# Kernel optimization log

Hardware: AMD Instinct MI355X
Metric: run time of the kernel (lower is better)

The kernel has to match this reference:

```python
import jax, jax.numpy as jnp
import numpy as np

DIM = 128      # channels C
HEADS = 4
HD = DIM // HEADS  # head_dim = 32
N = 128        # window tokens = 2*8*8
BW = 2048      # B_ = batch * num_windows
NP = 256       # sp_mask partitions
NW = 256       # shift-mask windows
TABLE = 675    # (2*2-1)*(2*8-1)*(2*8-1)
SCALE = HD ** -0.5


def setup_inputs() -> dict:
    key = jax.random.key(0)
    ks = jax.random.split(key, 8)
    x = jax.random.normal(ks[0], (BW, N, DIM), jnp.float32)
    rpi = jax.random.randint(ks[1], (N, N), 0, TABLE, dtype=jnp.int32)
    mask = jax.random.normal(ks[2], (NW, N, N), jnp.float32)
    sp_mask = jax.random.normal(ks[3], (NP, N, N), jnp.float32)
    w_qkv = jax.random.normal(ks[4], (3 * DIM, DIM), jnp.float32) * 0.02
    b_qkv = jnp.zeros((3 * DIM,), jnp.float32)
    bias_table = jax.random.normal(ks[5], (TABLE, HEADS), jnp.float32) * 0.02
    w_proj = jax.random.normal(ks[6], (DIM, DIM), jnp.float32) * 0.02
    b_proj = jnp.zeros((DIM,), jnp.float32)
    return {"x": x, "rpi": rpi, "mask": mask, "sp_mask": sp_mask,
            "w_qkv": w_qkv, "b_qkv": b_qkv, "bias_table": bias_table,
            "w_proj": w_proj, "b_proj": b_proj}


def reference(x, rpi, mask, sp_mask, w_qkv, b_qkv, bias_table, w_proj, b_proj):
    B_, Nn, C = x.shape
    # qkv projection -> (B_, N, 3, H, hd)
    qkv = (x @ w_qkv.T + b_qkv).reshape(B_, Nn, 3, HEADS, HD)
    q = qkv[:, :, 0].transpose(0, 2, 1, 3) * SCALE  # (B_, H, N, hd)
    k = qkv[:, :, 1].transpose(0, 2, 1, 3)
    v = qkv[:, :, 2].transpose(0, 2, 1, 3)
    attn = jnp.einsum('bhnd,bhmd->bhnm', q, k)  # (B_, H, N, N)
    # gathered relative position bias: (N, N, H) -> (H, N, N)
    rpb = bias_table[rpi].transpose(2, 0, 1)
    attn = attn + rpb[None]
    # additive sparse mask, broadcast over B_//nP groups and heads
    attn = (attn.reshape(B_ // NP, NP, HEADS, Nn, Nn)
            + sp_mask[None, :, None]).reshape(B_, HEADS, Nn, Nn)
    # additive shift mask, broadcast over B_//nW groups and heads
    attn = (attn.reshape(B_ // NW, NW, HEADS, Nn, Nn)
            + mask[None, :, None]).reshape(B_, HEADS, Nn, Nn)
    attn = jax.nn.softmax(attn, axis=-1)
    out = jnp.einsum('bhnm,bhmd->bnhd', attn, v).reshape(B_, Nn, C)
    return out @ w_proj.T + b_proj
```

## Files before the change

### kernel.cpp

```cpp
#include <hip/hip_runtime.h>

typedef short v8s __attribute__((ext_vector_type(8)));
typedef float v4f __attribute__((ext_vector_type(4)));

#define MFMA16(a, b, c) __builtin_amdgcn_mfma_f32_16x16x32_bf16(a, b, c, 0, 0, 0)

__device__ __forceinline__ unsigned short f2b(float f) {
  union { float f; unsigned int i; } v;
  v.f = f;
  unsigned int x = v.i;
  return (unsigned short)((x + 0x7fffu + ((x >> 16) & 1u)) >> 16);
}
__device__ __forceinline__ v8s ldf8(const float* p) {
  float4 a = *(const float4*)p;
  float4 b = *(const float4*)(p + 4);
  union { v8s v; unsigned short u[8]; } r;
  r.u[0] = f2b(a.x); r.u[1] = f2b(a.y); r.u[2] = f2b(a.z); r.u[3] = f2b(a.w);
  r.u[4] = f2b(b.x); r.u[5] = f2b(b.y); r.u[6] = f2b(b.z); r.u[7] = f2b(b.w);
  return r.v;
}
__device__ __forceinline__ v8s ld16u(const unsigned short* p) {
  union { v8s v; ushort4 h[2]; } u;
  u.h[0] = *(const ushort4*)(p);
  u.h[1] = *(const ushort4*)(p + 4);
  return u.v;
}

#define SCALE 0.17677669529663687f
#define LOG2E 1.4426950408889634f
#define QSCALE (SCALE * LOG2E)

#define WS_RPB 16777216
#define WS_WQH 17039360
#define WS_WPH 17137664

__global__ __launch_bounds__(256)
void conv_w(const float* __restrict__ wq, const float* __restrict__ wp,
            unsigned short* __restrict__ wqh, unsigned short* __restrict__ wph) {
  int i = blockIdx.x * 256 + threadIdx.x;
  if (i < 384 * 128) wqh[i] = f2b(wq[i]);
  else wph[i - 384 * 128] = f2b(wp[i - 384 * 128]);
}

__global__ __launch_bounds__(256)
void build_bias(const float* __restrict__ mask, const float* __restrict__ sp,
                const int* __restrict__ rpi, const float* __restrict__ btab,
                float* __restrict__ msum, float* __restrict__ rpb) {
  const int wgrp = blockIdx.x, tid = threadIdx.x;
  const float* mk = mask + (size_t)wgrp * 16384;
  const float* sk = sp + (size_t)wgrp * 16384;
  float* ot = msum + (size_t)wgrp * 16384;
  for (int it = 0; it < 16; ++it) {
    int i = (tid + 256 * it) * 4;
    float4 a = *(const float4*)(mk + i);
    float4 b = *(const float4*)(sk + i);
    float4 s;
    s.x = (a.x + b.x) * LOG2E; s.y = (a.y + b.y) * LOG2E;
    s.z = (a.z + b.z) * LOG2E; s.w = (a.w + b.w) * LOG2E;
    *(float4*)(ot + i) = s;
  }
  int e = wgrp * 256 + tid;
  int hh = e >> 14, r = e & 16383;
  rpb[e] = btab[rpi[r] * 4 + hh] * LOG2E;
}

__global__ __launch_bounds__(256, 4)
void attn_kernel(const float* __restrict__ xg,
                 const unsigned short* __restrict__ wqh,
                 const float* __restrict__ bq,
                 const float* __restrict__ msum,
                 const float* __restrict__ rpb,
                 float* __restrict__ o_ws) {
  __shared__ alignas(16) unsigned char smem[17664];
  unsigned short* kss = (unsigned short*)smem;
  unsigned short* vs  = (unsigned short*)(smem + 9216);

  const int tid = threadIdx.x;
  const int wv = tid >> 6;
  const int lane = tid & 63;
  const int qd = lane >> 4;
  const int t16 = lane & 15;

  const int idx = blockIdx.x;
  const int wgrp = idx >> 5;
  const int rem = idx & 31;
  const int h = rem >> 3;
  const int b = (rem & 7) * 256 + wgrp;

  const float* xb = xg + (size_t)b * 16384;
  v8s bx[2][4];
  for (int nt = 0; nt < 2; ++nt)
    for (int ks = 0; ks < 4; ++ks) {
      int n = 32 * wv + nt * 16 + t16;
      bx[nt][ks] = ldf8(xb + n * 128 + ks * 32 + 8 * qd);
    }

  v4f accqk[4][2];
  for (int jt = 0; jt < 4; ++jt)
    for (int nt = 0; nt < 2; ++nt) accqk[jt][nt] = v4f{0.f, 0.f, 0.f, 0.f};
  for (int jt = 0; jt < 4; ++jt) {
    int wbase = (jt < 2) ? (h * 32 + jt * 16) : (128 + h * 32 + (jt - 2) * 16);
    for (int ks = 0; ks < 4; ++ks) {
      v8s a = *(const v8s*)(wqh + (wbase + t16) * 128 + ks * 32 + 8 * qd);
      for (int nt = 0; nt < 2; ++nt)
        accqk[jt][nt] = MFMA16(a, bx[nt][ks], accqk[jt][nt]);
    }
  }
  v4f accv[2][2];
  for (int rt = 0; rt < 2; ++rt)
    for (int ct = 0; ct < 2; ++ct) accv[rt][ct] = v4f{0.f, 0.f, 0.f, 0.f};
  for (int ct = 0; ct < 2; ++ct)
    for (int ks = 0; ks < 4; ++ks) {
      v8s bw = *(const v8s*)(wqh + (256 + h * 32 + ct * 16 + t16) * 128 + ks * 32 + 8 * qd);
      for (int rt = 0; rt < 2; ++rt)
        accv[rt][ct] = MFMA16(bx[rt][ks], bw, accv[rt][ct]);
    }

  for (int jt = 2; jt < 4; ++jt)
    for (int nt = 0; nt < 2; ++nt) {
      int n = 32 * wv + nt * 16 + t16;
      ushort4 pk;
      float v0 = accqk[jt][nt][0] + bq[128 + h * 32 + (jt - 2) * 16 + 4 * qd + 0];
      float v1 = accqk[jt][nt][1] + bq[128 + h * 32 + (jt - 2) * 16 + 4 * qd + 1];
      float v2 = accqk[jt][nt][2] + bq[128 + h * 32 + (jt - 2) * 16 + 4 * qd + 2];
      float v3 = accqk[jt][nt][3] + bq[128 + h * 32 + (jt - 2) * 16 + 4 * qd + 3];
      pk.x = f2b(v0); pk.y = f2b(v1); pk.z = f2b(v2); pk.w = f2b(v3);
      *(ushort4*)(kss + n * 36 + (jt - 2) * 16 + 4 * qd) = pk;
    }
  for (int ct = 0; ct < 2; ++ct) {
    int d = ct * 16 + t16;
    float bv = bq[256 + h * 32 + d];
    for (int rt = 0; rt < 2; ++rt) {
      ushort4 pk;
      pk.x = f2b(accv[rt][ct][0] + bv);
      pk.y = f2b(accv[rt][ct][1] + bv);
      pk.z = f2b(accv[rt][ct][2] + bv);
      pk.w = f2b(accv[rt][ct][3] + bv);
      *(ushort4*)(vs + d * 132 + 32 * wv + rt * 16 + 4 * qd) = pk;
    }
  }

  unsigned int qpk[2][2][2];
  for (int jt = 0; jt < 2; ++jt)
    for (int nt = 0; nt < 2; ++nt) {
      float vv[4];
      for (int r = 0; r < 4; ++r)
        vv[r] = (accqk[jt][nt][r] + bq[h * 32 + jt * 16 + 4 * qd + r]) * QSCALE;
      qpk[jt][nt][0] = (unsigned int)f2b(vv[0]) | ((unsigned int)f2b(vv[1]) << 16);
      qpk[jt][nt][1] = (unsigned int)f2b(vv[2]) | ((unsigned int)f2b(vv[3]) << 16);
    }
  const int srcA = ((qd & 1) << 5) + t16;
  const bool hiq = qd >= 2;
  v8s aq[2];
  for (int rt = 0; rt < 2; ++rt) {
    union { v8s v; unsigned int d[4]; } u;
    unsigned int a0 = __shfl((int)qpk[0][rt][0], srcA, 64);
    unsigned int b0 = __shfl((int)qpk[1][rt][0], srcA, 64);
    unsigned int a1 = __shfl((int)qpk[0][rt][1], srcA, 64);
    unsigned int b1 = __shfl((int)qpk[1][rt][1], srcA, 64);
    unsigned int a2 = __shfl((int)qpk[0][rt][0], srcA + 16, 64);
    unsigned int b2 = __shfl((int)qpk[1][rt][0], srcA + 16, 64);
    unsigned int a3 = __shfl((int)qpk[0][rt][1], srcA + 16, 64);
    unsigned int b3 = __shfl((int)qpk[1][rt][1], srcA + 16, 64);
    u.d[0] = hiq ? b0 : a0;
    u.d[1] = hiq ? b1 : a1;
    u.d[2] = hiq ? b2 : a2;
    u.d[3] = hiq ? b3 : a3;
    aq[rt] = u.v;
  }
  __syncthreads();

  v4f sa[2][8];
  const v4f zero4 = {0.f, 0.f, 0.f, 0.f};
  for (int ct = 0; ct < 8; ++ct) {
    v8s bk = ld16u(kss + (ct * 16 + t16) * 36 + 8 * qd);
    for (int nt = 0; nt < 2; ++nt)
      sa[nt][ct] = MFMA16(bk, aq[nt], zero4);
  }
  {
    const float* mt = msum + (size_t)wgrp * 16384;
    const float* rb = rpb + (size_t)h * 16384;
    for (int nt = 0; nt < 2; ++nt) {
      int n = 32 * wv + nt * 16 + t16;
      const float* pm = mt + n * 128;
      const float* pr = rb + n * 128;
      for (int ct = 0; ct < 8; ++ct) {
        float4 b1 = *(const float4*)(pm + ct * 16 + 4 * qd);
        float4 b2 = *(const float4*)(pr + ct * 16 + 4 * qd);
        sa[nt][ct][0] += b1.x + b2.x;
        sa[nt][ct][1] += b1.y + b2.y;
        sa[nt][ct][2] += b1.z + b2.z;
        sa[nt][ct][3] += b1.w + b2.w;
      }
    }
  }
  float pinv[2];
  for (int nt = 0; nt < 2; ++nt) {
    float m0 = sa[nt][0][0];
    for (int ct = 0; ct < 8; ++ct)
      for (int r = 0; r < 4; ++r) m0 = fmaxf(m0, sa[nt][ct][r]);
    m0 = fmaxf(m0, __shfl_xor(m0, 16));
    m0 = fmaxf(m0, __shfl_xor(m0, 32));
    for (int ct = 0; ct < 8; ++ct)
      for (int r = 0; r < 4; ++r)
        sa[nt][ct][r] = exp2f(sa[nt][ct][r] - m0);
    float s0 = 0.f;
    for (int ct = 0; ct < 8; ++ct)
      for (int r = 0; r < 4; ++r) s0 += sa[nt][ct][r];
    s0 += __shfl_xor(s0, 16);
    s0 += __shfl_xor(s0, 32);
    pinv[nt] = 1.0f / s0;
  }

  v8s av[2][4];
  for (int rt = 0; rt < 2; ++rt)
    for (int ks = 0; ks < 4; ++ks)
      av[rt][ks] = ld16u(vs + (rt * 16 + t16) * 132 + ks * 32 + 8 * qd);

  const int srcP0 = ((qd & 1) << 5) + t16;
  const bool hip2 = qd >= 2;
  for (int nt = 0; nt < 2; ++nt) {
    unsigned int pkd[8][2];
    for (int ct = 0; ct < 8; ++ct) {
      pkd[ct][0] = (unsigned int)f2b(sa[nt][ct][0]) | ((unsigned int)f2b(sa[nt][ct][1]) << 16);
      pkd[ct][1] = (unsigned int)f2b(sa[nt][ct][2]) | ((unsigned int)f2b(sa[nt][ct][3]) << 16);
    }
    v8s bp[4];
    for (int ks = 0; ks < 4; ++ks) {
      union { v8s v; unsigned int d[4]; } u;
      unsigned int a0 = __shfl((int)pkd[2 * ks][0], srcP0, 64);
      unsigned int b0 = __shfl((int)pkd[2 * ks + 1][0], srcP0, 64);
      unsigned int a1 = __shfl((int)pkd[2 * ks][1], srcP0, 64);
      unsigned int b1 = __shfl((int)pkd[2 * ks + 1][1], srcP0, 64);
      unsigned int a2 = __shfl((int)pkd[2 * ks][0], srcP0 + 16, 64);
      unsigned int b2 = __shfl((int)pkd[2 * ks + 1][0], srcP0 + 16, 64);
      unsigned int a3 = __shfl((int)pkd[2 * ks][1], srcP0 + 16, 64);
      unsigned int b3 = __shfl((int)pkd[2 * ks + 1][1], srcP0 + 16, 64);
      u.d[0] = hip2 ? b0 : a0;
      u.d[1] = hip2 ? b1 : a1;
      u.d[2] = hip2 ? b2 : a2;
      u.d[3] = hip2 ? b3 : a3;
      bp[ks] = u.v;
    }
    v4f oa[2] = {zero4, zero4};
    for (int ks = 0; ks < 4; ++ks)
      for (int rt = 0; rt < 2; ++rt)
        oa[rt] = MFMA16(av[rt][ks], bp[ks], oa[rt]);
    int n = 32 * wv + nt * 16 + t16;
    float s = pinv[nt];
    for (int rt = 0; rt < 2; ++rt) {
      int cbase = h * 32 + rt * 16 + 4 * qd;
      float4 pk;
      pk.x = oa[rt][0] * s;
      pk.y = oa[rt][1] * s;
      pk.z = oa[rt][2] * s;
      pk.w = oa[rt][3] * s;
      *(float4*)(o_ws + ((size_t)(b * 128 + n)) * 128 + cbase) = pk;
    }
  }
}

__global__ __launch_bounds__(256, 4)
void proj_kernel(const unsigned short* __restrict__ wph,
                 const float* __restrict__ bpj,
                 float* __restrict__ out) {
  const int tid = threadIdx.x;
  const int wv = tid >> 6;
  const int lane = tid & 63;
  const int qd = lane >> 4;
  const int t16 = lane & 15;
  const size_t row0 = (size_t)blockIdx.x * 128;
  const float* src = out + row0 * 128;

  v8s bo[2][4];
  for (int ct = 0; ct < 2; ++ct)
    for (int ks = 0; ks < 4; ++ks) {
      int n = 32 * wv + ct * 16 + t16;
      bo[ct][ks] = ldf8(src + n * 128 + ks * 32 + 8 * qd);
    }
  v4f acc[8][2];
  for (int rt = 0; rt < 8; ++rt)
    for (int ct = 0; ct < 2; ++ct) acc[rt][ct] = v4f{0.f, 0.f, 0.f, 0.f};
  for (int rt = 0; rt < 8; ++rt)
    for (int ks = 0; ks < 4; ++ks) {
      v8s a = *(const v8s*)(wph + (rt * 16 + t16) * 128 + ks * 32 + 8 * qd);
      for (int ct = 0; ct < 2; ++ct)
        acc[rt][ct] = MFMA16(a, bo[ct][ks], acc[rt][ct]);
    }
  for (int rt = 0; rt < 8; ++rt) {
    float4 bj = *(const float4*)(bpj + rt * 16 + 4 * qd);
    for (int ct = 0; ct < 2; ++ct) {
      int n = 32 * wv + ct * 16 + t16;
      float4 pk;
      pk.x = acc[rt][ct][0] + bj.x;
      pk.y = acc[rt][ct][1] + bj.y;
      pk.z = acc[rt][ct][2] + bj.z;
      pk.w = acc[rt][ct][3] + bj.w;
      *(float4*)(out + (row0 + n) * 128 + rt * 16 + 4 * qd) = pk;
    }
  }
}

extern "C" void kernel_launch(void* const* d_in, const int* in_sizes, int n_in,
                              void* d_out, int out_size, void* d_ws, size_t ws_size,
                              hipStream_t stream) {
  (void)in_sizes; (void)n_in; (void)out_size; (void)ws_size;
  const float* xg   = (const float*)d_in[0];
  const int*   rpi  = (const int*)d_in[1];
  const float* mask = (const float*)d_in[2];
  const float* sp   = (const float*)d_in[3];
  const float* wq   = (const float*)d_in[4];
  const float* bq   = (const float*)d_in[5];
  const float* btab = (const float*)d_in[6];
  const float* wp   = (const float*)d_in[7];
  const float* bpj  = (const float*)d_in[8];
  float* out = (float*)d_out;

  float* msum = (float*)d_ws;
  float* rpb  = (float*)((char*)d_ws + WS_RPB);
  unsigned short* wqh = (unsigned short*)((char*)d_ws + WS_WQH);
  unsigned short* wph = (unsigned short*)((char*)d_ws + WS_WPH);

  conv_w<<<256, 256, 0, stream>>>(wq, wp, wqh, wph);
  build_bias<<<256, 256, 0, stream>>>(mask, sp, rpi, btab, msum, rpb);
  attn_kernel<<<8192, 256, 0, stream>>>(xg, wqh, bq, msum, rpb, out);
  proj_kernel<<<2048, 256, 0, stream>>>(wph, bpj, out);
}
```

Measured before the change: 553.0 us.

## Fuse attention and output projection into one per-window kernel with shared x tile

Merges the attention and projection kernels into one 1024-thread block per window, where 16 waves cover 4 heads by 4 row strips. The x tile is converted to bf16 once into swizzled LDS and shared across heads instead of being reloaded per head. The attention output stays in LDS as bf16 for the projection GEMM, removing the fp32 intermediate round trip through global memory. It also switches to hardware packed bf16 conversion and padded LDS strides. The cost is about 108KB of LDS per block, which limits occupancy to one block per CU, plus an extra rounding of the attention output to bf16 and scalar (non-vectorised) output stores.

```diff
diff --git a/kernel.cpp b/kernel.cpp
--- a/kernel.cpp
+++ b/kernel.cpp
@@ -11,19 +11,10 @@
   unsigned int x = v.i;
   return (unsigned short)((x + 0x7fffu + ((x >> 16) & 1u)) >> 16);
 }
-__device__ __forceinline__ v8s ldf8(const float* p) {
-  float4 a = *(const float4*)p;
-  float4 b = *(const float4*)(p + 4);
-  union { v8s v; unsigned short u[8]; } r;
-  r.u[0] = f2b(a.x); r.u[1] = f2b(a.y); r.u[2] = f2b(a.z); r.u[3] = f2b(a.w);
-  r.u[4] = f2b(b.x); r.u[5] = f2b(b.y); r.u[6] = f2b(b.z); r.u[7] = f2b(b.w);
-  return r.v;
-}
-__device__ __forceinline__ v8s ld16u(const unsigned short* p) {
-  union { v8s v; ushort4 h[2]; } u;
-  u.h[0] = *(const ushort4*)(p);
-  u.h[1] = *(const ushort4*)(p + 4);
-  return u.v;
+__device__ __forceinline__ unsigned int cvtpk(float lo, float hi) {
+  unsigned int r;
+  asm("v_cvt_pk_bf16_f32 %0, %1, %2" : "=v"(r) : "v"(lo), "v"(hi));
+  return r;
 }
 
 #define SCALE 0.17677669529663687f
@@ -64,35 +55,55 @@
   rpb[e] = btab[rpi[r] * 4 + hh] * LOG2E;
 }
 
-__global__ __launch_bounds__(256, 4)
-void attn_kernel(const float* __restrict__ xg,
-                 const unsigned short* __restrict__ wqh,
-                 const float* __restrict__ bq,
-                 const float* __restrict__ msum,
-                 const float* __restrict__ rpb,
-                 float* __restrict__ o_ws) {
-  __shared__ alignas(16) unsigned char smem[17664];
-  unsigned short* kss = (unsigned short*)smem;
-  unsigned short* vs  = (unsigned short*)(smem + 9216);
+__global__ __launch_bounds__(1024, 4)
+void attn_fused(const float* __restrict__ xg,
+                const unsigned short* __restrict__ wqh,
+                const float* __restrict__ bq,
+                const float* __restrict__ msum,
+                const float* __restrict__ rpb,
+                const unsigned short* __restrict__ wph,
+                const float* __restrict__ bpj,
+                float* __restrict__ out) {
+  __shared__ alignas(16) unsigned char smem[110592];
+  unsigned short* xs = (unsigned short*)smem;
+  unsigned short* os = (unsigned short*)smem;
 
   const int tid = threadIdx.x;
-  const int wv = tid >> 6;
+  const int wid = tid >> 6;
+  const int s = wid & 3;
+  const int h = wid >> 2;
   const int lane = tid & 63;
   const int qd = lane >> 4;
   const int t16 = lane & 15;
 
   const int idx = blockIdx.x;
-  const int wgrp = idx >> 5;
-  const int rem = idx & 31;
-  const int h = rem >> 3;
-  const int b = (rem & 7) * 256 + wgrp;
-
-  const float* xb = xg + (size_t)b * 16384;
+  const int wgrp = idx >> 3;
+  const int b = (idx & 7) * 256 + wgrp;
+
+  unsigned short* kss = (unsigned short*)(smem + 34816 + h * 10240);
+  unsigned short* vs  = (unsigned short*)(smem + 75776 + h * 8704);
+
+  {
+    const float* src = xg + (size_t)b * 16384;
+    for (int it = 0; it < 2; ++it) {
+      int gl = tid + 1024 * it;
+      int row = gl >> 4, g = gl & 15;
+      const float4* s4 = (const float4*)(src + row * 128 + g * 8);
+      float4 a = s4[0], c = s4[1];
+      union { int4 v; unsigned int d[4]; } pk;
+      pk.d[0] = cvtpk(a.x, a.y); pk.d[1] = cvtpk(a.z, a.w);
+      pk.d[2] = cvtpk(c.x, c.y); pk.d[3] = cvtpk(c.z, c.w);
+      *(int4*)(xs + row * 128 + ((g ^ (row & 15)) << 3)) = pk.v;
+    }
+  }
+  __syncthreads();
+
   v8s bx[2][4];
   for (int nt = 0; nt < 2; ++nt)
     for (int ks = 0; ks < 4; ++ks) {
-      int n = 32 * wv + nt * 16 + t16;
-      bx[nt][ks] = ldf8(xb + n * 128 + ks * 32 + 8 * qd);
+      int n = 32 * s + nt * 16 + t16;
+      int g = ks * 4 + qd;
+      bx[nt][ks] = *(const v8s*)(xs + n * 128 + ((g ^ (n & 15)) << 3));
     }
 
   v4f accqk[4][2];
@@ -118,36 +129,34 @@
 
   for (int jt = 2; jt < 4; ++jt)
     for (int nt = 0; nt < 2; ++nt) {
-      int n = 32 * wv + nt * 16 + t16;
-      ushort4 pk;
-      float v0 = accqk[jt][nt][0] + bq[128 + h * 32 + (jt - 2) * 16 + 4 * qd + 0];
-      float v1 = accqk[jt][nt][1] + bq[128 + h * 32 + (jt - 2) * 16 + 4 * qd + 1];
-      float v2 = accqk[jt][nt][2] + bq[128 + h * 32 + (jt - 2) * 16 + 4 * qd + 2];
-      float v3 = accqk[jt][nt][3] + bq[128 + h * 32 + (jt - 2) * 16 + 4 * qd + 3];
-      pk.x = f2b(v0); pk.y = f2b(v1); pk.z = f2b(v2); pk.w = f2b(v3);
-      *(ushort4*)(kss + n * 36 + (jt - 2) * 16 + 4 * qd) = pk;
+      int n = 32 * s + nt * 16 + t16;
+      int bb = 128 + h * 32 + (jt - 2) * 16 + 4 * qd;
+      uint2 pk;
+      pk.x = cvtpk(accqk[jt][nt][0] + bq[bb + 0], accqk[jt][nt][1] + bq[bb + 1]);
+      pk.y = cvtpk(accqk[jt][nt][2] + bq[bb + 2], accqk[jt][nt][3] + bq[bb + 3]);
+      *(uint2*)(kss + n * 40 + (jt - 2) * 16 + 4 * qd) = pk;
     }
   for (int ct = 0; ct < 2; ++ct) {
     int d = ct * 16 + t16;
     float bv = bq[256 + h * 32 + d];
     for (int rt = 0; rt < 2; ++rt) {
-      ushort4 pk;
-      pk.x = f2b(accv[rt][ct][0] + bv);
-      pk.y = f2b(accv[rt][ct][1] + bv);
-      pk.z = f2b(accv[rt][ct][2] + bv);
-      pk.w = f2b(accv[rt][ct][3] + bv);
-      *(ushort4*)(vs + d * 132 + 32 * wv + rt * 16 + 4 * qd) = pk;
+      uint2 pk;
+      pk.x = cvtpk(accv[rt][ct][0] + bv, accv[rt][ct][1] + bv);
+      pk.y = cvtpk(accv[rt][ct][2] + bv, accv[rt][ct][3] + bv);
+      *(uint2*)(vs + d * 136 + 32 * s + rt * 16 + 4 * qd) = pk;
     }
   }
 
   unsigned int qpk[2][2][2];
   for (int jt = 0; jt < 2; ++jt)
     for (int nt = 0; nt < 2; ++nt) {
-      float vv[4];
-      for (int r = 0; r < 4; ++r)
-        vv[r] = (accqk[jt][nt][r] + bq[h * 32 + jt * 16 + 4 * qd + r]) * QSCALE;
-      qpk[jt][nt][0] = (unsigned int)f2b(vv[0]) | ((unsigned int)f2b(vv[1]) << 16);
-      qpk[jt][nt][1] = (unsigned int)f2b(vv[2]) | ((unsigned int)f2b(vv[3]) << 16);
+      int bb = h * 32 + jt * 16 + 4 * qd;
+      float v0 = (accqk[jt][nt][0] + bq[bb + 0]) * QSCALE;
+      float v1 = (accqk[jt][nt][1] + bq[bb + 1]) * QSCALE;
+      float v2 = (accqk[jt][nt][2] + bq[bb + 2]) * QSCALE;
+      float v3 = (accqk[jt][nt][3] + bq[bb + 3]) * QSCALE;
+      qpk[jt][nt][0] = cvtpk(v0, v1);
+      qpk[jt][nt][1] = cvtpk(v2, v3);
     }
   const int srcA = ((qd & 1) << 5) + t16;
   const bool hiq = qd >= 2;
@@ -173,7 +182,7 @@
   v4f sa[2][8];
   const v4f zero4 = {0.f, 0.f, 0.f, 0.f};
   for (int ct = 0; ct < 8; ++ct) {
-    v8s bk = ld16u(kss + (ct * 16 + t16) * 36 + 8 * qd);
+    v8s bk = *(const v8s*)(kss + (ct * 16 + t16) * 40 + 8 * qd);
     for (int nt = 0; nt < 2; ++nt)
       sa[nt][ct] = MFMA16(bk, aq[nt], zero4);
   }
@@ -181,7 +190,7 @@
     const float* mt = msum + (size_t)wgrp * 16384;
     const float* rb = rpb + (size_t)h * 16384;
     for (int nt = 0; nt < 2; ++nt) {
-      int n = 32 * wv + nt * 16 + t16;
+      int n = 32 * s + nt * 16 + t16;
       const float* pm = mt + n * 128;
       const float* pr = rb + n * 128;
       for (int ct = 0; ct < 8; ++ct) {
@@ -215,15 +224,15 @@
   v8s av[2][4];
   for (int rt = 0; rt < 2; ++rt)
     for (int ks = 0; ks < 4; ++ks)
-      av[rt][ks] = ld16u(vs + (rt * 16 + t16) * 132 + ks * 32 + 8 * qd);
+      av[rt][ks] = *(const v8s*)(vs + (rt * 16 + t16) * 136 + ks * 32 + 8 * qd);
 
   const int srcP0 = ((qd & 1) << 5) + t16;
   const bool hip2 = qd >= 2;
   for (int nt = 0; nt < 2; ++nt) {
     unsigned int pkd[8][2];
     for (int ct = 0; ct < 8; ++ct) {
-      pkd[ct][0] = (unsigned int)f2b(sa[nt][ct][0]) | ((unsigned int)f2b(sa[nt][ct][1]) << 16);
-      pkd[ct][1] = (unsigned int)f2b(sa[nt][ct][2]) | ((unsigned int)f2b(sa[nt][ct][3]) << 16);
+      pkd[ct][0] = cvtpk(sa[nt][ct][0], sa[nt][ct][1]);
+      pkd[ct][1] = cvtpk(sa[nt][ct][2], sa[nt][ct][3]);
     }
     v8s bp[4];
     for (int ks = 0; ks < 4; ++ks) {
@@ -246,57 +255,36 @@
     for (int ks = 0; ks < 4; ++ks)
       for (int rt = 0; rt < 2; ++rt)
         oa[rt] = MFMA16(av[rt][ks], bp[ks], oa[rt]);
-    int n = 32 * wv + nt * 16 + t16;
-    float s = pinv[nt];
+    int n = 32 * s + nt * 16 + t16;
+    float sv = pinv[nt];
     for (int rt = 0; rt < 2; ++rt) {
-      int cbase = h * 32 + rt * 16 + 4 * qd;
-      float4 pk;
-      pk.x = oa[rt][0] * s;
-      pk.y = oa[rt][1] * s;
-      pk.z = oa[rt][2] * s;
-      pk.w = oa[rt][3] * s;
-      *(float4*)(o_ws + ((size_t)(b * 128 + n)) * 128 + cbase) = pk;
-    }
-  }
-}
-
-__global__ __launch_bounds__(256, 4)
-void proj_kernel(const unsigned short* __restrict__ wph,
-                 const float* __restrict__ bpj,
-                 float* __restrict__ out) {
-  const int tid = threadIdx.x;
-  const int wv = tid >> 6;
-  const int lane = tid & 63;
-  const int qd = lane >> 4;
-  const int t16 = lane & 15;
-  const size_t row0 = (size_t)blockIdx.x * 128;
-  const float* src = out + row0 * 128;
-
-  v8s bo[2][4];
-  for (int ct = 0; ct < 2; ++ct)
-    for (int ks = 0; ks < 4; ++ks) {
-      int n = 32 * wv + ct * 16 + t16;
-      bo[ct][ks] = ldf8(src + n * 128 + ks * 32 + 8 * qd);
-    }
-  v4f acc[8][2];
-  for (int rt = 0; rt < 8; ++rt)
-    for (int ct = 0; ct < 2; ++ct) acc[rt][ct] = v4f{0.f, 0.f, 0.f, 0.f};
-  for (int rt = 0; rt < 8; ++rt)
-    for (int ks = 0; ks < 4; ++ks) {
-      v8s a = *(const v8s*)(wph + (rt * 16 + t16) * 128 + ks * 32 + 8 * qd);
-      for (int ct = 0; ct < 2; ++ct)
-        acc[rt][ct] = MFMA16(a, bo[ct][ks], acc[rt][ct]);
-    }
-  for (int rt = 0; rt < 8; ++rt) {
-    float4 bj = *(const float4*)(bpj + rt * 16 + 4 * qd);
-    for (int ct = 0; ct < 2; ++ct) {
-      int n = 32 * wv + ct * 16 + t16;
-      float4 pk;
-      pk.x = acc[rt][ct][0] + bj.x;
-      pk.y = acc[rt][ct][1] + bj.y;
-      pk.z = acc[rt][ct][2] + bj.z;
-      pk.w = acc[rt][ct][3] + bj.w;
-      *(float4*)(out + (row0 + n) * 128 + rt * 16 + 4 * qd) = pk;
+      uint2 pk;
+      pk.x = cvtpk(oa[rt][0] * sv, oa[rt][1] * sv);
+      pk.y = cvtpk(oa[rt][2] * sv, oa[rt][3] * sv);
+      *(uint2*)(os + n * 136 + h * 32 + rt * 16 + 4 * qd) = pk;
+    }
+  }
+  __syncthreads();
+
+  {
+    const int tn = wid >> 1;
+    const int tc0 = (wid & 1) * 4;
+    v8s ao[4];
+    for (int ks = 0; ks < 4; ++ks)
+      ao[ks] = *(const v8s*)(os + (tn * 16 + t16) * 136 + ks * 32 + 8 * qd);
+    for (int tc = 0; tc < 4; ++tc) {
+      int co = (tc0 + tc) * 16;
+      v4f acc = zero4;
+      for (int ks = 0; ks < 4; ++ks) {
+        v8s bwp = *(const v8s*)(wph + (co + t16) * 128 + ks * 32 + 8 * qd);
+        acc = MFMA16(ao[ks], bwp, acc);
+      }
+      float bj = bpj[co + t16];
+      size_t rowb = (size_t)b * 128 + tn * 16 + 4 * qd;
+      out[(rowb + 0) * 128 + co + t16] = acc[0] + bj;
+      out[(rowb + 1) * 128 + co + t16] = acc[1] + bj;
+      out[(rowb + 2) * 128 + co + t16] = acc[2] + bj;
+      out[(rowb + 3) * 128 + co + t16] = acc[3] + bj;
     }
   }
 }
@@ -323,6 +311,5 @@
 
   conv_w<<<256, 256, 0, stream>>>(wq, wp, wqh, wph);
   build_bias<<<256, 256, 0, stream>>>(mask, sp, rpi, btab, msum, rpb);
-  attn_kernel<<<8192, 256, 0, stream>>>(xg, wqh, bq, msum, rpb, out);
-  proj_kernel<<<2048, 256, 0, stream>>>(wph, bpj, out);
-}
+  attn_fused<<<2048, 1024, 0, stream>>>(xg, wqh, bq, msum, rpb, wph, bpj, out);
+}
```

Measured after the change: 542.8 us. About the same (-1.8%).
